# Performance work log

Measured on AMD Instinct MI355X. Metric: run time of the kernel, lower is better.

Reference implementation:

```python
import jax, jax.numpy as jnp
import numpy as np
from jax import lax

COMMITMENT_COST = 0.25
NUM_EMB = 512
LATENT = 32


def _conv(x, w, b):
    # Conv2d(kernel=4, stride=2, padding=1), NCHW / OIHW
    y = lax.conv_general_dilated(x, w, window_strides=(2, 2),
                                 padding=((1, 1), (1, 1)),
                                 dimension_numbers=('NCHW', 'OIHW', 'NCHW'))
    return y + b[None, :, None, None]


def _deconv(x, w, b):
    # ConvTranspose2d(kernel=4, stride=2, padding=1); torch weight is [in, out, kh, kw].
    # Equivalent: input-dilated conv with flipped kernel, padding = k-1-p = 2.
    wf = jnp.flip(w, (2, 3)).transpose(1, 0, 2, 3)  # -> OIHW
    y = lax.conv_general_dilated(x, wf, window_strides=(1, 1),
                                 padding=((2, 2), (2, 2)),
                                 lhs_dilation=(2, 2),
                                 dimension_numbers=('NCHW', 'OIHW', 'NCHW'))
    return y + b[None, :, None, None]


def _vq(z, emb):
    # z: [B, C, H, W] -> NHWC
    zp = jnp.transpose(z, (0, 2, 3, 1))          # [B,H,W,C]
    flat = zp.reshape(-1, LATENT)                # [N,C]
    d = (jnp.sum(flat * flat, axis=1, keepdims=True)
         + jnp.sum(emb * emb, axis=1)
         - 2.0 * flat @ emb.T)                   # [N,K]
    idx = jnp.argmin(d, axis=1)                  # [N]
    q = emb[idx].reshape(zp.shape)               # gather == one_hot @ emb
    e_loss = jnp.mean((lax.stop_gradient(q) - zp) ** 2)
    q_loss = jnp.mean((q - lax.stop_gradient(zp)) ** 2)
    vq_loss = q_loss + COMMITMENT_COST * e_loss
    q_st = zp + lax.stop_gradient(q - zp)        # straight-through
    return jnp.transpose(q_st, (0, 3, 1, 2)), vq_loss, idx


def setup_inputs() -> dict:
    key = jax.random.key(0)
    ks = jax.random.split(key, 16)
    s = 0.05
    inp = {
        'x':  jax.random.uniform(ks[0], (128, 3, 128, 128), jnp.float32),
        'w1': jax.random.normal(ks[1], (32, 3, 4, 4), jnp.float32) * s,
        'b1': jax.random.normal(ks[2], (32,), jnp.float32) * s,
        'w2': jax.random.normal(ks[3], (64, 32, 4, 4), jnp.float32) * s,
        'b2': jax.random.normal(ks[4], (64,), jnp.float32) * s,
        'w3': jax.random.normal(ks[5], (LATENT, 64, 4, 4), jnp.float32) * s,
        'b3': jax.random.normal(ks[6], (LATENT,), jnp.float32) * s,
        'emb': jax.random.uniform(ks[7], (NUM_EMB, LATENT), jnp.float32,
                                  minval=-1.0 / NUM_EMB, maxval=1.0 / NUM_EMB),
        'd1': jax.random.normal(ks[8], (LATENT, 64, 4, 4), jnp.float32) * s,
        'db1': jax.random.normal(ks[9], (64,), jnp.float32) * s,
        'd2': jax.random.normal(ks[10], (64, 32, 4, 4), jnp.float32) * s,
        'db2': jax.random.normal(ks[11], (32,), jnp.float32) * s,
        'd3': jax.random.normal(ks[12], (32, 3, 4, 4), jnp.float32) * s,
        'db3': jax.random.normal(ks[13], (3,), jnp.float32) * s,
    }
    return inp


def reference(x, w1, b1, w2, b2, w3, b3, emb, d1, db1, d2, db2, d3, db3):
    # encoder
    h = jax.nn.relu(_conv(x, w1, b1))
    h = jax.nn.relu(_conv(h, w2, b2))
    z = _conv(h, w3, b3)                 # [B, LATENT, 16, 16]
    # vector quantization
    z_q, vq_loss, _ = _vq(z, emb)
    # decoder
    g = jax.nn.relu(_deconv(z_q, d1, db1))
    g = jax.nn.relu(_deconv(g, d2, db2))
    x_recon = jax.nn.sigmoid(_deconv(g, d3, db3))
    recon_loss = jnp.mean((x_recon - x) ** 2)
    return x_recon, recon_loss, vq_loss
```

## Files before the change

kernel.cpp:

```cpp
#include <hip/hip_runtime.h>
#include <math.h>

#define NEMB 512
#define LAT 32

typedef unsigned short u16;
typedef unsigned int u32;
typedef __attribute__((ext_vector_type(8))) short bf16x8;
typedef __attribute__((ext_vector_type(4))) float f32x4;

__device__ __forceinline__ u16 f2b(float f) {
    unsigned u = __builtin_bit_cast(unsigned, f);
    return (u16)((u + 0x7fffu + ((u >> 16) & 1u)) >> 16);
}
__device__ __forceinline__ float b2f(u16 h) {
    unsigned u = ((unsigned)h) << 16;
    return __builtin_bit_cast(float, u);
}
__device__ __forceinline__ float b2f_lo(u32 u) { return __builtin_bit_cast(float, u << 16); }
__device__ __forceinline__ float b2f_hi(u32 u) { return __builtin_bit_cast(float, u & 0xffff0000u); }

union V16 { uint4 u; u16 s[8]; };
union V8  { uint2 u; u16 s[4]; };

static const size_t OFF_H1  = 0;
static const size_t OFF_H2  = 33554432;
static const size_t OFF_Z   = 50331648;
static const size_t OFF_ZQ  = 52428800;
static const size_t OFF_W2T = 54525952;
static const size_t OFF_W3T = 54591488;
static const size_t OFF_D1T = 54657024;
static const size_t OFF_D2T = 54722560;
static const size_t OFF_ACC = 54804480;
static const size_t OFF_E2  = 54808576;
static const size_t OFF_W1T = 54810624;
static const size_t OFF_XB  = 54814720;

__global__ __launch_bounds__(256)
void prep_kernel(const float* __restrict__ w2, const float* __restrict__ w3,
                 const float* __restrict__ d1, const float* __restrict__ d2,
                 const float* __restrict__ emb, const float* __restrict__ w1,
                 u16* __restrict__ w2t, u16* __restrict__ w3t, u16* __restrict__ d1t,
                 u16* __restrict__ d2t, u16* __restrict__ w1t,
                 float* __restrict__ accum, float* __restrict__ e2) {
    int t = blockIdx.x * 256 + threadIdx.x;
    if (t < 32768) {
        int ci = t & 31; int t2 = t >> 5; int co = t2 & 63; int tau = t2 >> 6;
        w2t[t] = f2b(w2[((size_t)co * 32 + ci) * 16 + tau]);
    } else if (t < 65536) {
        int u = t - 32768;
        int ci = u & 63; int t2 = u >> 6; int co = t2 & 31; int tau = t2 >> 5;
        w3t[u] = f2b(w3[((size_t)co * 64 + ci) * 16 + tau]);
    } else if (t < 98304) {
        int u = t - 65536;
        int ci = u & 31; int t2 = u >> 5; int co = t2 & 63; int s = t2 >> 6;
        int ry = (s >> 3) & 1, rx = (s >> 2) & 1, a = (s >> 1) & 1, b = s & 1;
        int ky = ((ry + 1) & 1) + 2 * a, kx = ((rx + 1) & 1) + 2 * b;
        d1t[u] = f2b(d1[((size_t)ci * 64 + co) * 16 + ky * 4 + kx]);
    } else if (t < 131072) {
        int u = t - 98304;
        int ci = u & 63; int t2 = u >> 6; int co = t2 & 31; int s = t2 >> 5;
        int ry = (s >> 3) & 1, rx = (s >> 2) & 1, a = (s >> 1) & 1, b = s & 1;
        int ky = ((ry + 1) & 1) + 2 * a, kx = ((rx + 1) & 1) + 2 * b;
        d2t[u] = f2b(d2[((size_t)ci * 32 + co) * 16 + ky * 4 + kx]);
    } else if (t < 131584) {
        int u = t - 131072;
        float s = 0.f;
        #pragma unroll
        for (int c = 0; c < LAT; ++c) { float e = emb[u * LAT + c]; s = fmaf(e, e, s); }
        e2[u] = s;
    } else if (t < 132096) {
        accum[t - 131584] = 0.f;
    } else if (t < 134144) {
        int u = t - 132096;
        int k = u & 31; int co = (u >> 5) & 31; int c = u >> 10;
        int kyl = k >> 4, kx = (k >> 2) & 3, ch = k & 3;
        w1t[u] = (ch < 3) ? f2b(w1[((size_t)(co * 3 + ch) * 4 + (2 * c + kyl)) * 4 + kx])
                          : (u16)0;
    }
}

__global__ __launch_bounds__(256)
void xb_conv(const float* __restrict__ x, u16* __restrict__ xb) {
    int t = blockIdx.x * 256 + threadIdx.x;
    int xx = t % 130; int t2 = t / 130;
    int yy = t2 % 130; int n = t2 / 130;
    V8 o; o.u = (uint2){0, 0};
    if (xx >= 1 && xx <= 128 && yy >= 1 && yy <= 128) {
        size_t base = ((size_t)n * 3) * 16384 + (size_t)(yy - 1) * 128 + (xx - 1);
        o.s[0] = f2b(x[base]);
        o.s[1] = f2b(x[base + 16384]);
        o.s[2] = f2b(x[base + 32768]);
    }
    *(uint2*)&xb[(size_t)t * 4] = o.u;
}

__global__ __launch_bounds__(256)
void conv1_mfma(const u16* __restrict__ xb, const u16* __restrict__ w1t,
                const float* __restrict__ b1, u16* __restrict__ h1) {
    int bid = blockIdx.x;
    const int oyb = bid & 15; const int n = bid >> 4;
    const int tid = threadIdx.x, w = tid >> 6, lane = tid & 63;
    const int l15 = lane & 15, l4 = lane >> 4;
    const int oy = oyb * 4 + w;

    bf16x8 bf[2][2];
    #pragma unroll
    for (int c = 0; c < 2; ++c)
        #pragma unroll
        for (int cf = 0; cf < 2; ++cf)
            bf[c][cf] = *(const bf16x8*)&w1t[((size_t)(c * 32 + cf * 16 + l15)) * 32 + l4 * 8];

    f32x4 acc[4][2];
    #pragma unroll
    for (int f = 0; f < 4; ++f)
        #pragma unroll
        for (int cf = 0; cf < 2; ++cf) {
            float bv = b1[cf * 16 + l15];
            acc[f][cf] = (f32x4){bv, bv, bv, bv};
        }

    #pragma unroll
    for (int c = 0; c < 2; ++c) {
        const int row = 2 * oy + 2 * c + (l4 >> 1);
        #pragma unroll
        for (int f = 0; f < 4; ++f) {
            const int col = 2 * (f * 16 + l15) + (l4 & 1) * 2;
            bf16x8 a = *(const bf16x8*)&xb[(((size_t)n * 130 + row) * 130 + col) * 4];
            acc[f][0] = __builtin_amdgcn_mfma_f32_16x16x32_bf16(a, bf[c][0], acc[f][0], 0, 0, 0);
            acc[f][1] = __builtin_amdgcn_mfma_f32_16x16x32_bf16(a, bf[c][1], acc[f][1], 0, 0, 0);
        }
    }

    #pragma unroll
    for (int f = 0; f < 4; ++f)
        #pragma unroll
        for (int cf = 0; cf < 2; ++cf)
            #pragma unroll
            for (int rg = 0; rg < 4; ++rg) {
                int ox = f * 16 + l4 * 4 + rg;
                h1[(((size_t)n * 64 + oy) * 64 + ox) * 32 + cf * 16 + l15] =
                    f2b(fmaxf(acc[f][cf][rg], 0.f));
            }
}

template <int CI, int CO, int HI, int WI, bool RELU>
__global__ __launch_bounds__(256)
void mfma_conv(const u16* __restrict__ xin, const u16* __restrict__ wt,
               const float* __restrict__ bias, u16* __restrict__ out) {
    constexpr int HO = HI / 2, WO = WI / 2;
    constexpr int BCOLS = (WO < 32) ? WO : 32;
    constexpr int XC = 2 * BCOLS + 2;
    constexpr int NCOLF = BCOLS / 16, NCOF = CO / 16, NCC = CI / 32;
    constexpr int CPU8 = CI / 8;
    __shared__ u16 sx[10 * XC * CI];

    int bid = blockIdx.x;
    constexpr int NBY = HO / 4, NTX = WO / BCOLS;
    const int tx = bid % NTX; bid /= NTX;
    const int by = bid % NBY; const int n = bid / NBY;
    const int oy0 = by * 4, ox0 = tx * BCOLS;
    const int tid = threadIdx.x, w = tid >> 6, lane = tid & 63;
    const int l15 = lane & 15, l4 = lane >> 4;

    const int iyb = 2 * oy0 - 1, ixb = 2 * ox0 - 1;
    for (int u = tid; u < 10 * XC * CPU8; u += 256) {
        int c8 = u % CPU8; int t2 = u / CPU8;
        int xc = t2 % XC; int r = t2 / XC;
        int iy = iyb + r, ix = ixb + xc;
        uint4 v = {0, 0, 0, 0};
        if (iy >= 0 && iy < HI && ix >= 0 && ix < WI)
            v = *(const uint4*)&xin[(((size_t)n * HI + iy) * WI + ix) * CI + c8 * 8];
        int byte = ((r * XC + xc) * CI + c8 * 8) * 2;
        byte ^= ((xc >> 1) & 7) << 4;
        *(uint4*)&sx[byte >> 1] = v;
    }
    __syncthreads();

    f32x4 acc[NCOLF][NCOF];
    #pragma unroll
    for (int pf = 0; pf < NCOLF; ++pf)
        #pragma unroll
        for (int cf = 0; cf < NCOF; ++cf) {
            float bv = bias[cf * 16 + l15];
            acc[pf][cf] = (f32x4){bv, bv, bv, bv};
        }

    #pragma unroll 2
    for (int tau = 0; tau < 16; ++tau) {
        const int ky = tau >> 2, kx = tau & 3;
        const int r = 2 * w + ky;
        #pragma unroll
        for (int cc = 0; cc < NCC; ++cc) {
            bf16x8 b[NCOF];
            #pragma unroll
            for (int cf = 0; cf < NCOF; ++cf)
                b[cf] = *(const bf16x8*)&wt[((size_t)(tau * CO + cf * 16 + l15)) * CI + cc * 32 + l4 * 8];
            bf16x8 a[NCOLF];
            #pragma unroll
            for (int pf = 0; pf < NCOLF; ++pf) {
                int xc = 2 * (pf * 16 + l15) + kx;
                int byte = ((r * XC + xc) * CI + cc * 32 + l4 * 8) * 2;
                byte ^= ((xc >> 1) & 7) << 4;
                a[pf] = *(const bf16x8*)&sx[byte >> 1];
            }
            #pragma unroll
            for (int pf = 0; pf < NCOLF; ++pf)
                #pragma unroll
                for (int cf = 0; cf < NCOF; ++cf)
                    acc[pf][cf] = __builtin_amdgcn_mfma_f32_16x16x32_bf16(
                        a[pf], b[cf], acc[pf][cf], 0, 0, 0);
        }
    }

    const int oy = oy0 + w;
    #pragma unroll
    for (int pf = 0; pf < NCOLF; ++pf)
        #pragma unroll
        for (int cf = 0; cf < NCOF; ++cf)
            #pragma unroll
            for (int rg = 0; rg < 4; ++rg) {
                int ox = ox0 + pf * 16 + l4 * 4 + rg;
                float v = acc[pf][cf][rg];
                if (RELU) v = fmaxf(v, 0.f);
                out[(((size_t)n * HO + oy) * WO + ox) * CO + cf * 16 + l15] = f2b(v);
            }
}

template <int CI, int CO, int HI, int WI>
__global__ __launch_bounds__(256)
void mfma_deconv2w(const u16* __restrict__ xin, const u16* __restrict__ wt,
                   const float* __restrict__ bias, u16* __restrict__ out) {
    constexpr int HO = 2 * HI, WO = 2 * WI;
    constexpr int BCOLS = (WI < 32) ? WI : 32;
    constexpr int XC = BCOLS + 2;
    constexpr int NCOLF = BCOLS / 16, NCOF = CO / 16, NCC = CI / 32;
    constexpr int CPU8 = CI / 8;
    __shared__ u16 sx[4 * XC * CI];

    int bid = blockIdx.x;
    constexpr int NBY = HI / 2, NTX = WI / BCOLS;
    const int tx = bid % NTX; bid /= NTX;
    const int by = bid % NBY; const int n = bid / NBY;
    const int q0 = by * 2, r0 = tx * BCOLS;
    const int tid = threadIdx.x, w = tid >> 6, lane = tid & 63;
    const int l15 = lane & 15, l4 = lane >> 4;
    const int ry = w & 1, qw = w >> 1;

    const int qb0 = q0 - 1;
    for (int u = tid; u < 4 * XC * CPU8; u += 256) {
        int c8 = u % CPU8; int t2 = u / CPU8;
        int xc = t2 % XC; int r = t2 / XC;
        int iy = qb0 + r, ix = r0 - 1 + xc;
        uint4 v = {0, 0, 0, 0};
        if (iy >= 0 && iy < HI && ix >= 0 && ix < WI)
            v = *(const uint4*)&xin[(((size_t)n * HI + iy) * WI + ix) * CI + c8 * 8];
        int byte = ((r * XC + xc) * CI + c8 * 8) * 2;
        byte ^= (xc & 7) << 4;
        *(uint4*)&sx[byte >> 1] = v;
    }
    __syncthreads();

    f32x4 acc[2][NCOLF][NCOF];
    #pragma unroll
    for (int rx = 0; rx < 2; ++rx)
        #pragma unroll
        for (int pf = 0; pf < NCOLF; ++pf)
            #pragma unroll
            for (int cf = 0; cf < NCOF; ++cf) {
                float bv = bias[cf * 16 + l15];
                acc[rx][pf][cf] = (f32x4){bv, bv, bv, bv};
            }

    #pragma unroll
    for (int rx = 0; rx < 2; ++rx) {
        #pragma unroll
        for (int cc = 0; cc < NCC; ++cc) {
            bf16x8 b[4][NCOF];
            #pragma unroll
            for (int tap = 0; tap < 4; ++tap) {
                const int sidx = ry * 8 + rx * 4 + tap;
                #pragma unroll
                for (int cf = 0; cf < NCOF; ++cf)
                    b[tap][cf] = *(const bf16x8*)&wt[((size_t)(sidx * CO + cf * 16 + l15)) * CI + cc * 32 + l4 * 8];
            }
            #pragma unroll
            for (int tap = 0; tap < 4; ++tap) {
                const int a_ = tap >> 1, b_ = tap & 1;
                const int r = ry + qw + 1 - a_;
                bf16x8 a[NCOLF];
                #pragma unroll
                for (int pf = 0; pf < NCOLF; ++pf) {
                    int xc = pf * 16 + l15 + rx - b_ + 1;
                    int byte = ((r * XC + xc) * CI + cc * 32 + l4 * 8) * 2;
                    byte ^= (xc & 7) << 4;
                    a[pf] = *(const bf16x8*)&sx[byte >> 1];
                }
                #pragma unroll
                for (int pf = 0; pf < NCOLF; ++pf)
                    #pragma unroll
                    for (int cf = 0; cf < NCOF; ++cf)
                        acc[rx][pf][cf] = __builtin_amdgcn_mfma_f32_16x16x32_bf16(
                            a[pf], b[tap][cf], acc[rx][pf][cf], 0, 0, 0);
            }
        }
    }

    const int oy = 2 * (q0 + qw) + ry;
    #pragma unroll
    for (int rx = 0; rx < 2; ++rx)
        #pragma unroll
        for (int pf = 0; pf < NCOLF; ++pf)
            #pragma unroll
            for (int cf = 0; cf < NCOF; ++cf)
                #pragma unroll
                for (int rg = 0; rg < 4; ++rg) {
                    int ox = 2 * (r0 + pf * 16 + l4 * 4 + rg) + rx;
                    float v = fmaxf(acc[rx][pf][cf][rg], 0.f);
                    out[(((size_t)n * HO + oy) * WO + ox) * CO + cf * 16 + l15] = f2b(v);
                }
}

__global__ __launch_bounds__(256)
void deconv3_direct(const u16* __restrict__ g2, const float* __restrict__ d3,
                    const float* __restrict__ db3, float* __restrict__ out,
                    const float* __restrict__ ref, float* __restrict__ buckets) {
    __shared__ u32 sxp[16 * 412];
    __shared__ float sw[32 * 3 * 16];
    int bid = blockIdx.x;
    const int ty = bid & 15; const int n = bid >> 4;
    const int tid = threadIdx.x;
    const int w = tid >> 6, lane = tid & 63;
    const int row = (w & 1) + 4 * (w >> 1) + 2 * (lane >> 5);
    const int cg = lane & 31;

    const int iy_org = ty * 4 - 1;

    for (int u = tid; u < 6 * 66 * 4; u += 256) {
        int c8 = u & 3; int pos = u >> 2;
        int col = pos % 66; int r = pos / 66;
        int iy = iy_org + r, ix = col - 1;
        uint4 v = {0, 0, 0, 0};
        if (iy >= 0 && iy < 64 && ix >= 0 && ix < 64)
            v = *(const uint4*)&g2[(((size_t)n * 64 + iy) * 64 + ix) * 32 + c8 * 8];
        int base = r * 68 + col;
        sxp[(c8 * 4 + 0) * 412 + base] = v.x;
        sxp[(c8 * 4 + 1) * 412 + base] = v.y;
        sxp[(c8 * 4 + 2) * 412 + base] = v.z;
        sxp[(c8 * 4 + 3) * 412 + base] = v.w;
    }
    for (int l = tid; l < 1536; l += 256) sw[l] = d3[l];
    __syncthreads();

    const int ky0 = (row + 1) & 1;
    const int iyA = ((row + 1 - ky0) >> 1) + 1;
    const int iyB = iyA - 1;
    const int q = cg * 2;

    float acc[3][4];
    #pragma unroll
    for (int co = 0; co < 3; ++co) {
        float b = db3[co];
        #pragma unroll
        for (int p = 0; p < 4; ++p) acc[co][p] = b;
    }

    #pragma unroll 1
    for (int c2 = 0; c2 < 16; ++c2) {
        uint4 hA = *(const uint4*)&sxp[c2 * 412 + iyA * 68 + q];
        uint4 hB = *(const uint4*)&sxp[c2 * 412 + iyB * 68 + q];
        u32 ta[4] = {hA.x, hA.y, hA.z, hA.w};
        u32 tb[4] = {hB.x, hB.y, hB.z, hB.w};
        #pragma unroll
        for (int cc = 0; cc < 2; ++cc) {
            const int ci = 2 * c2 + cc;
            float tA[4], tB[4];
            #pragma unroll
            for (int j = 0; j < 4; ++j) {
                tA[j] = cc ? b2f_hi(ta[j]) : b2f_lo(ta[j]);
                tB[j] = cc ? b2f_hi(tb[j]) : b2f_lo(tb[j]);
            }
            #pragma unroll
            for (int co = 0; co < 3; ++co) {
                const float4* wv = (const float4*)&sw[(ci * 3 + co) * 16];
                float4 wA = wv[ky0], wB = wv[ky0 + 2];
                #pragma unroll
                for (int p = 0; p < 4; ++p) {
                    const int A = (p + 3) >> 1;
                    const int B = (p + 1) >> 1;
                    float a = acc[co][p];
                    if (((p + 1) & 1) == 1) {
                        a = fmaf(tA[A], wA.y, a);
                        a = fmaf(tA[B], wA.w, a);
                        a = fmaf(tB[A], wB.y, a);
                        a = fmaf(tB[B], wB.w, a);
                    } else {
                        a = fmaf(tA[A], wA.x, a);
                        a = fmaf(tA[B], wA.z, a);
                        a = fmaf(tB[A], wB.x, a);
                        a = fmaf(tB[B], wB.z, a);
                    }
                    acc[co][p] = a;
                }
            }
        }
    }

    const int oy = ty * 8 + row, oxb = cg * 4;
    float lsum = 0.f;
    #pragma unroll
    for (int co = 0; co < 3; ++co) {
        size_t oi = (((size_t)n * 3 + co) * 128 + oy) * 128 + oxb;
        float4 rf = *(const float4*)&ref[oi];
        float4 st;
        st.x = 1.f / (1.f + __expf(-acc[co][0]));
        st.y = 1.f / (1.f + __expf(-acc[co][1]));
        st.z = 1.f / (1.f + __expf(-acc[co][2]));
        st.w = 1.f / (1.f + __expf(-acc[co][3]));
        *(float4*)&out[oi] = st;
        float d0 = st.x - rf.x, d1 = st.y - rf.y, d2 = st.z - rf.z, d3v = st.w - rf.w;
        lsum += d0 * d0 + d1 * d1 + d2 * d2 + d3v * d3v;
    }
    #pragma unroll
    for (int off = 32; off; off >>= 1) lsum += __shfl_down(lsum, off, 64);
    if ((tid & 63) == 0) atomicAdd(&buckets[blockIdx.x & 255], lsum);
}

__global__ __launch_bounds__(256)
void vq_mfma(const u16* __restrict__ z, const float* __restrict__ emb,
             const float* __restrict__ e2g, u16* __restrict__ zq,
             float* __restrict__ vq_buckets) {
    __shared__ u16 semb[NEMB * LAT];
    __shared__ float se2[NEMB];
    const int tid = threadIdx.x;

    for (int u = tid; u < 2048; u += 256) {
        int code = u >> 2, seg = u & 3;
        const float4* ep = (const float4*)&emb[code * 32 + seg * 8];
        float4 e0 = ep[0], e1 = ep[1];
        V16 o;
        o.s[0] = f2b(e0.x); o.s[1] = f2b(e0.y); o.s[2] = f2b(e0.z); o.s[3] = f2b(e0.w);
        o.s[4] = f2b(e1.x); o.s[5] = f2b(e1.y); o.s[6] = f2b(e1.z); o.s[7] = f2b(e1.w);
        int byte = (code * 64 + seg * 16) ^ ((code & 7) << 4);
        *(uint4*)((char*)semb + byte) = o.u;
    }
    if (tid < NEMB) se2[tid] = e2g[tid];
    __syncthreads();

    const int w = tid >> 6, lane = tid & 63;
    const int l15 = lane & 15, l4 = lane >> 4;
    const int rowbase = blockIdx.x * 64 + w * 16;

    bf16x8 a = *(const bf16x8*)&z[(size_t)(rowbase + l15) * LAT + l4 * 8];

    float best[4] = {1e30f, 1e30f, 1e30f, 1e30f};
    int   bidx[4] = {0, 0, 0, 0};
    #pragma unroll
    for (int f = 0; f < 32; ++f) {
        int byteb = ((f * 16 + l15) * 64 + l4 * 16) ^ ((l15 & 7) << 4);
        bf16x8 bfrag = *(const bf16x8*)((const char*)semb + byteb);
        f32x4 s = {0.f, 0.f, 0.f, 0.f};
        s = __builtin_amdgcn_mfma_f32_16x16x32_bf16(a, bfrag, s, 0, 0, 0);
        float e2c = se2[f * 16 + l15];
        int cidx = f * 16 + l15;
        #pragma unroll
        for (int j = 0; j < 4; ++j) {
            float d = fmaf(s[j], -2.f, e2c);
            bool lt = d < best[j];
            best[j] = lt ? d : best[j];
            bidx[j] = lt ? cidx : bidx[j];
        }
    }
    #pragma unroll
    for (int m = 1; m < 16; m <<= 1) {
        #pragma unroll
        for (int j = 0; j < 4; ++j) {
            float ob = __shfl_xor(best[j], m, 64);
            int   oi = __shfl_xor(bidx[j], m, 64);
            bool take = (ob < best[j]) || (ob == best[j] && oi < bidx[j]);
            best[j] = take ? ob : best[j];
            bidx[j] = take ? oi : bidx[j];
        }
    }
    const int r = lane >> 2;
    const int j0 = r & 3;
    int k = (j0 == 0) ? bidx[0] : (j0 == 1) ? bidx[1] : (j0 == 2) ? bidx[2] : bidx[3];
    const int seg = lane & 3;
    const float4* ep = (const float4*)&emb[k * LAT + seg * 8];
    float4 e0 = ep[0], e1 = ep[1];
    float ev[8] = {e0.x, e0.y, e0.z, e0.w, e1.x, e1.y, e1.z, e1.w};
    size_t zoff = (size_t)(rowbase + r) * LAT + seg * 8;
    V16 zr; zr.u = *(const uint4*)&z[zoff];
    V16 o;
    float local = 0.f;
    #pragma unroll
    for (int jj = 0; jj < 8; ++jj) {
        float dd = ev[jj] - b2f(zr.s[jj]);
        local = fmaf(dd, dd, local);
        o.s[jj] = f2b(ev[jj]);
    }
    *(uint4*)&zq[zoff] = o.u;
    #pragma unroll
    for (int off = 32; off; off >>= 1) local += __shfl_down(local, off, 64);
    if (lane == 0) atomicAdd(&vq_buckets[blockIdx.x & 255], local);
}

__global__ void finalize_kernel(const float* __restrict__ accum, float* __restrict__ out,
                                int out_size) {
    int tid = threadIdx.x;
    float v  = accum[tid];
    float vq = accum[256 + tid];
    #pragma unroll
    for (int off = 32; off; off >>= 1) {
        v  += __shfl_down(v, off, 64);
        vq += __shfl_down(vq, off, 64);
    }
    __shared__ float s[8];
    if ((tid & 63) == 0) { s[tid >> 6] = v; s[4 + (tid >> 6)] = vq; }
    __syncthreads();
    if (tid == 0) {
        float rt = s[0] + s[1] + s[2] + s[3];
        float qt = s[4] + s[5] + s[6] + s[7];
        out[out_size - 2] = rt / 6291456.f;
        out[out_size - 1] = 1.25f * qt / 1048576.f;
    }
}

extern "C" void kernel_launch(void* const* d_in, const int* in_sizes, int n_in,
                              void* d_out, int out_size, void* d_ws, size_t ws_size,
                              hipStream_t stream) {
    const float* x   = (const float*)d_in[0];
    const float* w1  = (const float*)d_in[1];
    const float* b1  = (const float*)d_in[2];
    const float* w2  = (const float*)d_in[3];
    const float* b2  = (const float*)d_in[4];
    const float* w3  = (const float*)d_in[5];
    const float* b3  = (const float*)d_in[6];
    const float* emb = (const float*)d_in[7];
    const float* d1  = (const float*)d_in[8];
    const float* db1 = (const float*)d_in[9];
    const float* d2  = (const float*)d_in[10];
    const float* db2 = (const float*)d_in[11];
    const float* d3  = (const float*)d_in[12];
    const float* db3 = (const float*)d_in[13];

    char* ws = (char*)d_ws;
    u16* h1  = (u16*)(ws + OFF_H1);
    u16* h2  = (u16*)(ws + OFF_H2);
    u16* zb  = (u16*)(ws + OFF_Z);
    u16* zqb = (u16*)(ws + OFF_ZQ);
    u16* w2t = (u16*)(ws + OFF_W2T);
    u16* w3t = (u16*)(ws + OFF_W3T);
    u16* d1t = (u16*)(ws + OFF_D1T);
    u16* d2t = (u16*)(ws + OFF_D2T);
    u16* w1t = (u16*)(ws + OFF_W1T);
    u16* xb  = (u16*)(ws + OFF_XB);
    float* acc = (float*)(ws + OFF_ACC);
    float* e2  = (float*)(ws + OFF_E2);
    float* out = (float*)d_out;

    prep_kernel<<<524, 256, 0, stream>>>(w2, w3, d1, d2, emb, w1,
                                         w2t, w3t, d1t, d2t, w1t, acc, e2);
    xb_conv<<<8450, 256, 0, stream>>>(x, xb);

    conv1_mfma<<<2048, 256, 0, stream>>>(xb, w1t, b1, h1);
    mfma_conv<32, 64, 64, 64, true ><<<1024, 256, 0, stream>>>(h1, w2t, b2, h2);
    mfma_conv<64, 32, 32, 32, false><<<512, 256, 0, stream>>>(h2, w3t, b3, zb);

    vq_mfma<<<512, 256, 0, stream>>>(zb, emb, e2, zqb, acc + 256);

    u16* g1 = h2; u16* g2 = h1;
    mfma_deconv2w<32, 64, 16, 16><<<1024, 256, 0, stream>>>(zqb, d1t, db1, g1);
    mfma_deconv2w<64, 32, 32, 32><<<2048, 256, 0, stream>>>(g1, d2t, db2, g2);
    deconv3_direct<<<2048, 256, 0, stream>>>(g2, d3, db3, out, x, acc);

    finalize_kernel<<<1, 256, 0, stream>>>(acc, out, out_size);
}
```

Before: 192.9 us.

## Merge prep and input-convert kernels; deconv blocks loop over two images with register prefetch

The weight-prep kernel and the input bf16 conversion kernel are merged into one launch, removing a kernel launch and the gap between them. The two MFMA deconvolution kernels now process two batch images per block, prefetching the next image's input tile into registers while the current one is computed. Weight loads are reused across the images and the block count is halved. This adds register pressure (launch bounds now ask for 3 blocks per CU) and gives fewer blocks in flight.

Result: slower. 226.5 us (+17.4%).

```diff
diff --git a/kernel.cpp b/kernel.cpp
--- a/kernel.cpp
+++ b/kernel.cpp
@@ -37,12 +37,27 @@
 static const size_t OFF_XB  = 54814720;
 
 __global__ __launch_bounds__(256)
-void prep_kernel(const float* __restrict__ w2, const float* __restrict__ w3,
-                 const float* __restrict__ d1, const float* __restrict__ d2,
-                 const float* __restrict__ emb, const float* __restrict__ w1,
-                 u16* __restrict__ w2t, u16* __restrict__ w3t, u16* __restrict__ d1t,
-                 u16* __restrict__ d2t, u16* __restrict__ w1t,
-                 float* __restrict__ accum, float* __restrict__ e2) {
+void prep_xb(const float* __restrict__ w2, const float* __restrict__ w3,
+             const float* __restrict__ d1, const float* __restrict__ d2,
+             const float* __restrict__ emb, const float* __restrict__ w1,
+             const float* __restrict__ x,
+             u16* __restrict__ w2t, u16* __restrict__ w3t, u16* __restrict__ d1t,
+             u16* __restrict__ d2t, u16* __restrict__ w1t, u16* __restrict__ xb,
+             float* __restrict__ accum, float* __restrict__ e2) {
+    if (blockIdx.x >= 524) {
+        int t = (blockIdx.x - 524) * 256 + threadIdx.x;
+        int xx = t % 130; int t2 = t / 130;
+        int yy = t2 % 130; int n = t2 / 130;
+        V8 o; o.u = (uint2){0, 0};
+        if (xx >= 1 && xx <= 128 && yy >= 1 && yy <= 128) {
+            size_t base = ((size_t)n * 3) * 16384 + (size_t)(yy - 1) * 128 + (xx - 1);
+            o.s[0] = f2b(x[base]);
+            o.s[1] = f2b(x[base + 16384]);
+            o.s[2] = f2b(x[base + 32768]);
+        }
+        *(uint2*)&xb[(size_t)t * 4] = o.u;
+        return;
+    }
     int t = blockIdx.x * 256 + threadIdx.x;
     if (t < 32768) {
         int ci = t & 31; int t2 = t >> 5; int co = t2 & 63; int tau = t2 >> 6;
@@ -81,21 +96,6 @@
 }
 
 __global__ __launch_bounds__(256)
-void xb_conv(const float* __restrict__ x, u16* __restrict__ xb) {
-    int t = blockIdx.x * 256 + threadIdx.x;
-    int xx = t % 130; int t2 = t / 130;
-    int yy = t2 % 130; int n = t2 / 130;
-    V8 o; o.u = (uint2){0, 0};
-    if (xx >= 1 && xx <= 128 && yy >= 1 && yy <= 128) {
-        size_t base = ((size_t)n * 3) * 16384 + (size_t)(yy - 1) * 128 + (xx - 1);
-        o.s[0] = f2b(x[base]);
-        o.s[1] = f2b(x[base + 16384]);
-        o.s[2] = f2b(x[base + 32768]);
-    }
-    *(uint2*)&xb[(size_t)t * 4] = o.u;
-}
-
-__global__ __launch_bounds__(256)
 void conv1_mfma(const u16* __restrict__ xb, const u16* __restrict__ w1t,
                 const float* __restrict__ b1, u16* __restrict__ h1) {
     int bid = blockIdx.x;
@@ -227,98 +227,132 @@
             }
 }
 
-template <int CI, int CO, int HI, int WI>
-__global__ __launch_bounds__(256)
-void mfma_deconv2w(const u16* __restrict__ xin, const u16* __restrict__ wt,
-                   const float* __restrict__ bias, u16* __restrict__ out) {
+template <int CI, int CO, int HI, int WI, int T>
+__global__ __launch_bounds__(256, 3)
+void mfma_deconv_nl(const u16* __restrict__ xin, const u16* __restrict__ wt,
+                    const float* __restrict__ bias, u16* __restrict__ out) {
     constexpr int HO = 2 * HI, WO = 2 * WI;
     constexpr int BCOLS = (WI < 32) ? WI : 32;
     constexpr int XC = BCOLS + 2;
     constexpr int NCOLF = BCOLS / 16, NCOF = CO / 16, NCC = CI / 32;
     constexpr int CPU8 = CI / 8;
+    constexpr int NSTG = 4 * XC * CPU8;
+    constexpr int NIT = (NSTG + 255) / 256;
+    constexpr size_t NSTRIDE = (size_t)HI * WI * CI;
     __shared__ u16 sx[4 * XC * CI];
 
     int bid = blockIdx.x;
     constexpr int NBY = HI / 2, NTX = WI / BCOLS;
     const int tx = bid % NTX; bid /= NTX;
-    const int by = bid % NBY; const int n = bid / NBY;
+    const int by = bid % NBY; const int np = bid / NBY;
     const int q0 = by * 2, r0 = tx * BCOLS;
     const int tid = threadIdx.x, w = tid >> 6, lane = tid & 63;
     const int l15 = lane & 15, l4 = lane >> 4;
     const int ry = w & 1, qw = w >> 1;
-
+    const int n0 = np * T;
     const int qb0 = q0 - 1;
-    for (int u = tid; u < 4 * XC * CPU8; u += 256) {
-        int c8 = u % CPU8; int t2 = u / CPU8;
+
+    int    s_byte[NIT];
+    size_t s_goff[NIT];
+    bool   s_ok[NIT];
+    #pragma unroll
+    for (int i = 0; i < NIT; ++i) {
+        int u = tid + i * 256;
+        bool valid = (u < NSTG);
+        int uu = valid ? u : 0;
+        int c8 = uu % CPU8; int t2 = uu / CPU8;
         int xc = t2 % XC; int r = t2 / XC;
         int iy = qb0 + r, ix = r0 - 1 + xc;
+        s_ok[i] = valid && iy >= 0 && iy < HI && ix >= 0 && ix < WI;
+        s_goff[i] = ((size_t)iy * WI + ix) * CI + c8 * 8;
+        int byte = ((r * XC + xc) * CI + c8 * 8) * 2;
+        s_byte[i] = byte ^ ((xc & 7) << 4);
+    }
+
+    uint4 sreg[NIT];
+    #pragma unroll
+    for (int i = 0; i < NIT; ++i) {
         uint4 v = {0, 0, 0, 0};
-        if (iy >= 0 && iy < HI && ix >= 0 && ix < WI)
-            v = *(const uint4*)&xin[(((size_t)n * HI + iy) * WI + ix) * CI + c8 * 8];
-        int byte = ((r * XC + xc) * CI + c8 * 8) * 2;
-        byte ^= (xc & 7) << 4;
-        *(uint4*)&sx[byte >> 1] = v;
-    }
-    __syncthreads();
-
-    f32x4 acc[2][NCOLF][NCOF];
-    #pragma unroll
-    for (int rx = 0; rx < 2; ++rx)
-        #pragma unroll
-        for (int pf = 0; pf < NCOLF; ++pf)
-            #pragma unroll
-            for (int cf = 0; cf < NCOF; ++cf) {
-                float bv = bias[cf * 16 + l15];
-                acc[rx][pf][cf] = (f32x4){bv, bv, bv, bv};
+        if (s_ok[i]) v = *(const uint4*)&xin[(size_t)n0 * NSTRIDE + s_goff[i]];
+        sreg[i] = v;
+    }
+
+    for (int t = 0; t < T; ++t) {
+        const int n = n0 + t;
+        __syncthreads();
+        #pragma unroll
+        for (int i = 0; i < NIT; ++i)
+            if (tid + i * 256 < NSTG) *(uint4*)&sx[s_byte[i] >> 1] = sreg[i];
+        __syncthreads();
+
+        if (t + 1 < T) {
+            #pragma unroll
+            for (int i = 0; i < NIT; ++i) {
+                uint4 v = {0, 0, 0, 0};
+                if (s_ok[i]) v = *(const uint4*)&xin[(size_t)(n + 1) * NSTRIDE + s_goff[i]];
+                sreg[i] = v;
             }
-
-    #pragma unroll
-    for (int rx = 0; rx < 2; ++rx) {
-        #pragma unroll
-        for (int cc = 0; cc < NCC; ++cc) {
-            bf16x8 b[4][NCOF];
-            #pragma unroll
-            for (int tap = 0; tap < 4; ++tap) {
-                const int sidx = ry * 8 + rx * 4 + tap;
+        }
+
+        f32x4 acc[2][NCOLF][NCOF];
+        #pragma unroll
+        for (int rx = 0; rx < 2; ++rx)
+            #pragma unroll
+            for (int pf = 0; pf < NCOLF; ++pf)
+                #pragma unroll
+                for (int cf = 0; cf < NCOF; ++cf) {
+                    float bv = bias[cf * 16 + l15];
+                    acc[rx][pf][cf] = (f32x4){bv, bv, bv, bv};
+                }
+
+        #pragma unroll
+        for (int rx = 0; rx < 2; ++rx) {
+            #pragma unroll
+            for (int cc = 0; cc < NCC; ++cc) {
+                bf16x8 b[4][NCOF];
+                #pragma unroll
+                for (int tap = 0; tap < 4; ++tap) {
+                    const int sidx = ry * 8 + rx * 4 + tap;
+                    #pragma unroll
+                    for (int cf = 0; cf < NCOF; ++cf)
+                        b[tap][cf] = *(const bf16x8*)&wt[((size_t)(sidx * CO + cf * 16 + l15)) * CI + cc * 32 + l4 * 8];
+                }
+                #pragma unroll
+                for (int tap = 0; tap < 4; ++tap) {
+                    const int a_ = tap >> 1, b_ = tap & 1;
+                    const int r = ry + qw + 1 - a_;
+                    bf16x8 a[NCOLF];
+                    #pragma unroll
+                    for (int pf = 0; pf < NCOLF; ++pf) {
+                        int xc = pf * 16 + l15 + rx - b_ + 1;
+                        int byte = ((r * XC + xc) * CI + cc * 32 + l4 * 8) * 2;
+                        byte ^= (xc & 7) << 4;
+                        a[pf] = *(const bf16x8*)&sx[byte >> 1];
+                    }
+                    #pragma unroll
+                    for (int pf = 0; pf < NCOLF; ++pf)
+                        #pragma unroll
+                        for (int cf = 0; cf < NCOF; ++cf)
+                            acc[rx][pf][cf] = __builtin_amdgcn_mfma_f32_16x16x32_bf16(
+                                a[pf], b[tap][cf], acc[rx][pf][cf], 0, 0, 0);
+                }
+            }
+        }
+
+        const int oy = 2 * (q0 + qw) + ry;
+        #pragma unroll
+        for (int rx = 0; rx < 2; ++rx)
+            #pragma unroll
+            for (int pf = 0; pf < NCOLF; ++pf)
                 #pragma unroll
                 for (int cf = 0; cf < NCOF; ++cf)
-                    b[tap][cf] = *(const bf16x8*)&wt[((size_t)(sidx * CO + cf * 16 + l15)) * CI + cc * 32 + l4 * 8];
-            }
-            #pragma unroll
-            for (int tap = 0; tap < 4; ++tap) {
-                const int a_ = tap >> 1, b_ = tap & 1;
-                const int r = ry + qw + 1 - a_;
-                bf16x8 a[NCOLF];
-                #pragma unroll
-                for (int pf = 0; pf < NCOLF; ++pf) {
-                    int xc = pf * 16 + l15 + rx - b_ + 1;
-                    int byte = ((r * XC + xc) * CI + cc * 32 + l4 * 8) * 2;
-                    byte ^= (xc & 7) << 4;
-                    a[pf] = *(const bf16x8*)&sx[byte >> 1];
-                }
-                #pragma unroll
-                for (int pf = 0; pf < NCOLF; ++pf)
                     #pragma unroll
-                    for (int cf = 0; cf < NCOF; ++cf)
-                        acc[rx][pf][cf] = __builtin_amdgcn_mfma_f32_16x16x32_bf16(
-                            a[pf], b[tap][cf], acc[rx][pf][cf], 0, 0, 0);
-            }
-        }
-    }
-
-    const int oy = 2 * (q0 + qw) + ry;
-    #pragma unroll
-    for (int rx = 0; rx < 2; ++rx)
-        #pragma unroll
-        for (int pf = 0; pf < NCOLF; ++pf)
-            #pragma unroll
-            for (int cf = 0; cf < NCOF; ++cf)
-                #pragma unroll
-                for (int rg = 0; rg < 4; ++rg) {
-                    int ox = 2 * (r0 + pf * 16 + l4 * 4 + rg) + rx;
-                    float v = fmaxf(acc[rx][pf][cf][rg], 0.f);
-                    out[(((size_t)n * HO + oy) * WO + ox) * CO + cf * 16 + l15] = f2b(v);
-                }
+                    for (int rg = 0; rg < 4; ++rg) {
+                        int ox = 2 * (r0 + pf * 16 + l4 * 4 + rg) + rx;
+                        float v = fmaxf(acc[rx][pf][cf][rg], 0.f);
+                        out[(((size_t)n * HO + oy) * WO + ox) * CO + cf * 16 + l15] = f2b(v);
+                    }
+    }
 }
 
 __global__ __launch_bounds__(256)
@@ -559,9 +593,8 @@
     float* e2  = (float*)(ws + OFF_E2);
     float* out = (float*)d_out;
 
-    prep_kernel<<<524, 256, 0, stream>>>(w2, w3, d1, d2, emb, w1,
-                                         w2t, w3t, d1t, d2t, w1t, acc, e2);
-    xb_conv<<<8450, 256, 0, stream>>>(x, xb);
+    prep_xb<<<524 + 8450, 256, 0, stream>>>(w2, w3, d1, d2, emb, w1, x,
+                                            w2t, w3t, d1t, d2t, w1t, xb, acc, e2);
 
     conv1_mfma<<<2048, 256, 0, stream>>>(xb, w1t, b1, h1);
     mfma_conv<32, 64, 64, 64, true ><<<1024, 256, 0, stream>>>(h1, w2t, b2, h2);
@@ -570,8 +603,8 @@
     vq_mfma<<<512, 256, 0, stream>>>(zb, emb, e2, zqb, acc + 256);
 
     u16* g1 = h2; u16* g2 = h1;
-    mfma_deconv2w<32, 64, 16, 16><<<1024, 256, 0, stream>>>(zqb, d1t, db1, g1);
-    mfma_deconv2w<64, 32, 32, 32><<<2048, 256, 0, stream>>>(g1, d2t, db2, g2);
+    mfma_deconv_nl<32, 64, 16, 16, 2><<<512, 256, 0, stream>>>(zqb, d1t, db1, g1);
+    mfma_deconv_nl<64, 32, 32, 32, 2><<<1024, 256, 0, stream>>>(g1, d2t, db2, g2);
     deconv3_direct<<<2048, 256, 0, stream>>>(g2, d3, db3, out, x, acc);
 
     finalize_kernel<<<1, 256, 0, stream>>>(acc, out, out_size);
```

## Stage deconv weights in LDS with per-parity blocks; fuse prep and input conversion

Applied to the files above, without the earlier changes.

The two MFMA deconvolution kernels now give each block a single output-row parity (blockIdx.y), with all four waves covering four input rows. Each block stages its 8 weight slices for that parity into swizzled LDS instead of reloading B fragments from global memory per wave. The halo tile grows to 5 rows, and the tap/cc loops are reordered to load B per tap. Separately, the prep and input bf16 conversion kernels are merged into one launch to drop a kernel boundary. In exchange, LDS per block grows, which may reduce occupancy, and each block now stages weight data it did not load before.

New measurement: 162.7 us. 1.19x faster.

```diff
diff --git a/kernel.cpp b/kernel.cpp
--- a/kernel.cpp
+++ b/kernel.cpp
@@ -37,12 +37,27 @@
 static const size_t OFF_XB  = 54814720;
 
 __global__ __launch_bounds__(256)
-void prep_kernel(const float* __restrict__ w2, const float* __restrict__ w3,
-                 const float* __restrict__ d1, const float* __restrict__ d2,
-                 const float* __restrict__ emb, const float* __restrict__ w1,
-                 u16* __restrict__ w2t, u16* __restrict__ w3t, u16* __restrict__ d1t,
-                 u16* __restrict__ d2t, u16* __restrict__ w1t,
-                 float* __restrict__ accum, float* __restrict__ e2) {
+void prep_xb(const float* __restrict__ w2, const float* __restrict__ w3,
+             const float* __restrict__ d1, const float* __restrict__ d2,
+             const float* __restrict__ emb, const float* __restrict__ w1,
+             const float* __restrict__ x,
+             u16* __restrict__ w2t, u16* __restrict__ w3t, u16* __restrict__ d1t,
+             u16* __restrict__ d2t, u16* __restrict__ w1t, u16* __restrict__ xb,
+             float* __restrict__ accum, float* __restrict__ e2) {
+    if (blockIdx.x >= 524) {
+        int t = (blockIdx.x - 524) * 256 + threadIdx.x;
+        int xx = t % 130; int t2 = t / 130;
+        int yy = t2 % 130; int n = t2 / 130;
+        V8 o; o.u = (uint2){0, 0};
+        if (xx >= 1 && xx <= 128 && yy >= 1 && yy <= 128) {
+            size_t base = ((size_t)n * 3) * 16384 + (size_t)(yy - 1) * 128 + (xx - 1);
+            o.s[0] = f2b(x[base]);
+            o.s[1] = f2b(x[base + 16384]);
+            o.s[2] = f2b(x[base + 32768]);
+        }
+        *(uint2*)&xb[(size_t)t * 4] = o.u;
+        return;
+    }
     int t = blockIdx.x * 256 + threadIdx.x;
     if (t < 32768) {
         int ci = t & 31; int t2 = t >> 5; int co = t2 & 63; int tau = t2 >> 6;
@@ -81,21 +96,6 @@
 }
 
 __global__ __launch_bounds__(256)
-void xb_conv(const float* __restrict__ x, u16* __restrict__ xb) {
-    int t = blockIdx.x * 256 + threadIdx.x;
-    int xx = t % 130; int t2 = t / 130;
-    int yy = t2 % 130; int n = t2 / 130;
-    V8 o; o.u = (uint2){0, 0};
-    if (xx >= 1 && xx <= 128 && yy >= 1 && yy <= 128) {
-        size_t base = ((size_t)n * 3) * 16384 + (size_t)(yy - 1) * 128 + (xx - 1);
-        o.s[0] = f2b(x[base]);
-        o.s[1] = f2b(x[base + 16384]);
-        o.s[2] = f2b(x[base + 32768]);
-    }
-    *(uint2*)&xb[(size_t)t * 4] = o.u;
-}
-
-__global__ __launch_bounds__(256)
 void conv1_mfma(const u16* __restrict__ xb, const u16* __restrict__ w1t,
                 const float* __restrict__ b1, u16* __restrict__ h1) {
     int bid = blockIdx.x;
@@ -229,29 +229,30 @@
 
 template <int CI, int CO, int HI, int WI>
 __global__ __launch_bounds__(256)
-void mfma_deconv2w(const u16* __restrict__ xin, const u16* __restrict__ wt,
-                   const float* __restrict__ bias, u16* __restrict__ out) {
+void mfma_deconv_wl(const u16* __restrict__ xin, const u16* __restrict__ wt,
+                    const float* __restrict__ bias, u16* __restrict__ out) {
     constexpr int HO = 2 * HI, WO = 2 * WI;
     constexpr int BCOLS = (WI < 32) ? WI : 32;
     constexpr int XC = BCOLS + 2;
     constexpr int NCOLF = BCOLS / 16, NCOF = CO / 16, NCC = CI / 32;
     constexpr int CPU8 = CI / 8;
-    __shared__ u16 sx[4 * XC * CI];
-
+    __shared__ u16 sx[5 * XC * CI];
+    __shared__ u16 swt[8 * CO * CI];
+
+    const int ry = blockIdx.y;
     int bid = blockIdx.x;
-    constexpr int NBY = HI / 2, NTX = WI / BCOLS;
+    constexpr int NBY = HI / 4, NTX = WI / BCOLS;
     const int tx = bid % NTX; bid /= NTX;
     const int by = bid % NBY; const int n = bid / NBY;
-    const int q0 = by * 2, r0 = tx * BCOLS;
+    const int q0 = by * 4, r0 = tx * BCOLS;
     const int tid = threadIdx.x, w = tid >> 6, lane = tid & 63;
     const int l15 = lane & 15, l4 = lane >> 4;
-    const int ry = w & 1, qw = w >> 1;
-
-    const int qb0 = q0 - 1;
-    for (int u = tid; u < 4 * XC * CPU8; u += 256) {
+
+    const int qb = q0 + ry - 1;
+    for (int u = tid; u < 5 * XC * CPU8; u += 256) {
         int c8 = u % CPU8; int t2 = u / CPU8;
         int xc = t2 % XC; int r = t2 / XC;
-        int iy = qb0 + r, ix = r0 - 1 + xc;
+        int iy = qb + r, ix = r0 - 1 + xc;
         uint4 v = {0, 0, 0, 0};
         if (iy >= 0 && iy < HI && ix >= 0 && ix < WI)
             v = *(const uint4*)&xin[(((size_t)n * HI + iy) * WI + ix) * CI + c8 * 8];
@@ -259,6 +260,15 @@
         byte ^= (xc & 7) << 4;
         *(uint4*)&sx[byte >> 1] = v;
     }
+    const u16* wts = wt + (size_t)(ry * 8) * CO * CI;
+    for (int u = tid; u < 8 * CO * CPU8; u += 256) {
+        int c8 = u % CPU8; int t2 = u / CPU8;
+        int co = t2 % CO; int l = t2 / CO;
+        uint4 v = *(const uint4*)&wts[((size_t)l * CO + co) * CI + c8 * 8];
+        int byte = ((l * CO + co) * CI + c8 * 8) * 2;
+        byte ^= (co & 7) << 4;
+        *(uint4*)&swt[byte >> 1] = v;
+    }
     __syncthreads();
 
     f32x4 acc[2][NCOLF][NCOF];
@@ -275,19 +285,19 @@
     #pragma unroll
     for (int rx = 0; rx < 2; ++rx) {
         #pragma unroll
-        for (int cc = 0; cc < NCC; ++cc) {
-            bf16x8 b[4][NCOF];
-            #pragma unroll
-            for (int tap = 0; tap < 4; ++tap) {
-                const int sidx = ry * 8 + rx * 4 + tap;
+        for (int tap = 0; tap < 4; ++tap) {
+            const int a_ = tap >> 1, b_ = tap & 1;
+            const int r = w + 1 - a_;
+            const int l = rx * 4 + tap;
+            #pragma unroll
+            for (int cc = 0; cc < NCC; ++cc) {
+                bf16x8 b[NCOF];
                 #pragma unroll
-                for (int cf = 0; cf < NCOF; ++cf)
-                    b[tap][cf] = *(const bf16x8*)&wt[((size_t)(sidx * CO + cf * 16 + l15)) * CI + cc * 32 + l4 * 8];
-            }
-            #pragma unroll
-            for (int tap = 0; tap < 4; ++tap) {
-                const int a_ = tap >> 1, b_ = tap & 1;
-                const int r = ry + qw + 1 - a_;
+                for (int cf = 0; cf < NCOF; ++cf) {
+                    int co = cf * 16 + l15;
+                    int byte = (((l * CO + co) * CI + cc * 32 + l4 * 8) * 2) ^ ((co & 7) << 4);
+                    b[cf] = *(const bf16x8*)((const char*)swt + byte);
+                }
                 bf16x8 a[NCOLF];
                 #pragma unroll
                 for (int pf = 0; pf < NCOLF; ++pf) {
@@ -301,12 +311,12 @@
                     #pragma unroll
                     for (int cf = 0; cf < NCOF; ++cf)
                         acc[rx][pf][cf] = __builtin_amdgcn_mfma_f32_16x16x32_bf16(
-                            a[pf], b[tap][cf], acc[rx][pf][cf], 0, 0, 0);
-            }
-        }
-    }
-
-    const int oy = 2 * (q0 + qw) + ry;
+                            a[pf], b[cf], acc[rx][pf][cf], 0, 0, 0);
+            }
+        }
+    }
+
+    const int oy = 2 * (q0 + w) + ry;
     #pragma unroll
     for (int rx = 0; rx < 2; ++rx)
         #pragma unroll
@@ -559,9 +569,8 @@
     float* e2  = (float*)(ws + OFF_E2);
     float* out = (float*)d_out;
 
-    prep_kernel<<<524, 256, 0, stream>>>(w2, w3, d1, d2, emb, w1,
-                                         w2t, w3t, d1t, d2t, w1t, acc, e2);
-    xb_conv<<<8450, 256, 0, stream>>>(x, xb);
+    prep_xb<<<524 + 8450, 256, 0, stream>>>(w2, w3, d1, d2, emb, w1, x,
+                                            w2t, w3t, d1t, d2t, w1t, xb, acc, e2);
 
     conv1_mfma<<<2048, 256, 0, stream>>>(xb, w1t, b1, h1);
     mfma_conv<32, 64, 64, 64, true ><<<1024, 256, 0, stream>>>(h1, w2t, b2, h2);
@@ -570,8 +579,8 @@
     vq_mfma<<<512, 256, 0, stream>>>(zb, emb, e2, zqb, acc + 256);
 
     u16* g1 = h2; u16* g2 = h1;
-    mfma_deconv2w<32, 64, 16, 16><<<1024, 256, 0, stream>>>(zqb, d1t, db1, g1);
-    mfma_deconv2w<64, 32, 32, 32><<<2048, 256, 0, stream>>>(g1, d2t, db2, g2);
+    mfma_deconv_wl<32, 64, 16, 16><<<dim3(512, 2), 256, 0, stream>>>(zqb, d1t, db1, g1);
+    mfma_deconv_wl<64, 32, 32, 32><<<dim3(1024, 2), 256, 0, stream>>>(g1, d2t, db2, g2);
     deconv3_direct<<<2048, 256, 0, stream>>>(g2, d3, db3, out, x, acc);
 
     finalize_kernel<<<1, 256, 0, stream>>>(acc, out, out_size);
```
